# Performance work log

Measured on AMD Instinct MI355X. Metric: run time of the kernel, lower is better.

The kernel has to match this reference:

```python
import jax, jax.numpy as jnp
import numpy as np

NEG_INF = -9e15
ALPHA = 0.2  # LeakyReLU negative slope


def setup_inputs() -> dict:
    key = jax.random.key(0)
    k1, k2, k3, k4 = jax.random.split(key, 4)
    N, F_in, F_out = 8192, 128, 64
    h = jax.random.normal(k1, (N, F_in), dtype=jnp.float32)
    adj = jax.random.randint(k2, (N, N), 0, 2, dtype=jnp.int32)
    W = jax.random.normal(k3, (F_in, F_out), dtype=jnp.float32) * (1.414 / np.sqrt(F_in))
    a = jax.random.normal(k4, (2 * F_out, 1), dtype=jnp.float32) * 0.1
    return {"h": h, "adj": adj, "W": W, "a": a}


def reference(h, adj, W, a):
    # Wh: [N, F_out]
    Wh = h @ W
    F_out = Wh.shape[1]
    # Decomposed additive score: cat([Wh_i, Wh_j]) @ a == Wh_i@a1 + Wh_j@a2.
    # Identical math to the original repeat/cat/mm, without the [N*N, 2F] blowup.
    s1 = Wh @ a[:F_out, 0]   # [N] source-side score
    s2 = Wh @ a[F_out:, 0]   # [N] target-side score
    e = jax.nn.leaky_relu(s1[:, None] + s2[None, :], negative_slope=ALPHA)  # [N, N]
    attention = jax.nn.softmax(jnp.where(adj > 0, e, NEG_INF), axis=1)
    # dropout is identity in eval mode
    h_prime = attention @ Wh  # [N, F_out]
    return (h_prime, attention)
```

## Files before the change

kernel.cpp:

```cpp
#include <hip/hip_runtime.h>

#define NN 8192
#define FIN 128
#define FOUT 64
#define NEGINF (-9e15f)
#define LALPHA 0.2f

typedef float f32x4 __attribute__((ext_vector_type(4)));
typedef float f32x2 __attribute__((ext_vector_type(2)));
typedef short short8 __attribute__((ext_vector_type(8)));
typedef unsigned long long ull;

__device__ __forceinline__ unsigned short f32_to_bf16(float x) {
  unsigned int u = __float_as_uint(x);
  u = (u + 0x7fffu + ((u >> 16) & 1u)) >> 16;
  return (unsigned short)u;
}
__device__ __forceinline__ float bf16_to_f32(unsigned short b) {
  return __uint_as_float(((unsigned int)b) << 16);
}

__global__ __launch_bounds__(256) void gat_prep(
    const float* __restrict__ h, const float* __restrict__ W,
    const float* __restrict__ a,
    float* __restrict__ s1g, float* __restrict__ s2g,
    unsigned short* __restrict__ whfh)
{
  __shared__ __align__(16) float Wl[FIN * FOUT];
  __shared__ __align__(16) float hl[16 * FIN];
  const int tid = threadIdx.x;
  const int i0 = blockIdx.x * 16;
  #pragma unroll
  for (int it = 0; it < 8; ++it) {
    int idx = (it * 256 + tid) * 4;
    *(f32x4*)&Wl[idx] = *(const f32x4*)&W[idx];
  }
  #pragma unroll
  for (int it = 0; it < 2; ++it) {
    int idx = (it * 256 + tid) * 4;
    *(f32x4*)&hl[idx] = *(const f32x4*)&h[(size_t)i0 * FIN + idx];
  }
  __syncthreads();
  const int r = tid >> 4;
  const int f0 = (tid & 15) * 4;
  f32x4 acc = {0.f, 0.f, 0.f, 0.f};
  #pragma unroll 8
  for (int k = 0; k < FIN; ++k) {
    float hv = hl[r * FIN + k];
    f32x4 wv = *(const f32x4*)&Wl[k * FOUT + f0];
    acc += hv * wv;
  }
  f32x4 a1v = *(const f32x4*)&a[f0];
  f32x4 a2v = *(const f32x4*)&a[FOUT + f0];
  float p1 = acc.x * a1v.x + acc.y * a1v.y + acc.z * a1v.z + acc.w * a1v.w;
  float p2 = acc.x * a2v.x + acc.y * a2v.y + acc.z * a2v.z + acc.w * a2v.w;
  #pragma unroll
  for (int d = 1; d < 16; d <<= 1) {
    p1 += __shfl_xor(p1, d, 16);
    p2 += __shfl_xor(p2, d, 16);
  }
  const int j = i0 + r;
  if ((tid & 15) == 0) { s1g[j] = p1; s2g[j] = p2; }
  const int kstep = j >> 5;
  const int lhi = (j >> 3) & 3;
  const int ein = j & 7;
  #pragma unroll
  for (int e = 0; e < 4; ++e) {
    int f = f0 + e;
    unsigned short hb = f32_to_bf16(acc[e]);
    int ln = lhi * 16 + (f & 15);
    whfh[(size_t)(kstep * 4 + (f >> 4)) * 512 + ln * 8 + ein] = hb;
  }
}

__global__ __launch_bounds__(512, 4) void gat_fused(
    const int* __restrict__ adj,
    const float* __restrict__ s1g, const float* __restrict__ s2g,
    const unsigned short* __restrict__ whfh,
    float* __restrict__ outh, float* __restrict__ outa)
{
  __shared__ __align__(16) float s2l[NN];
  __shared__ __align__(16) unsigned int maskl[16][258];
  __shared__ __align__(16) float red[4][1024];
  __shared__ float rowp[16][3];
  __shared__ float smaxl;
  const int tid = threadIdx.x;
  const int lane = tid & 63;
  const int wv = tid >> 6;
  const int i0 = blockIdx.x * 16;

  float lmax = -3.4e38f;
  #pragma unroll
  for (int it = 0; it < 4; ++it) {
    int idx = (it * 512 + tid) * 4;
    f32x4 v = *(const f32x4*)&s2g[idx];
    *(f32x4*)&s2l[idx] = v;
    lmax = fmaxf(fmaxf(fmaxf(lmax, v.x), fmaxf(v.y, v.z)), v.w);
  }
  #pragma unroll
  for (int d = 1; d < 64; d <<= 1) lmax = fmaxf(lmax, __shfl_xor(lmax, d));
  if (lane == 0) red[0][wv] = lmax;
  __syncthreads();
  if (tid == 0) {
    float m = red[0][0];
    #pragma unroll
    for (int w = 1; w < 8; ++w) m = fmaxf(m, red[0][w]);
    smaxl = m;
  }
  __syncthreads();
  const float smax = smaxl;

  {
    const int r0 = wv * 2, r1 = r0 + 1;
    const float s1a = s1g[i0 + r0];
    const float s1b = s1g[i0 + r1];
    const float za = s1a + smax, zb = s1b + smax;
    const float Ma = fmaxf(za, LALPHA * za);
    const float Mb = fmaxf(zb, LALPHA * zb);
    const int* __restrict__ ara = adj + (size_t)(i0 + r0) * NN;
    const int* __restrict__ arb = adj + (size_t)(i0 + r1) * NN;
    float la = 0.f, lb = 0.f;
    #pragma unroll 4
    for (int it = 0; it < 128; ++it) {
      int jj = it * 64 + lane;
      int a0 = __builtin_nontemporal_load(&ara[jj]);
      int a1 = __builtin_nontemporal_load(&arb[jj]);
      float sv = s2l[jj];
      ull b0 = __ballot(a0 > 0);
      ull b1 = __ballot(a1 > 0);
      float xa = s1a + sv; xa = fmaxf(xa, LALPHA * xa);
      float xb = s1b + sv; xb = fmaxf(xb, LALPHA * xb);
      float ea = __expf(xa - Ma);
      float eb = __expf(xb - Mb);
      la += (a0 > 0) ? ea : 0.f;
      lb += (a1 > 0) ? eb : 0.f;
      if (lane == 0) {
        *(ull*)&maskl[r0][it * 2] = b0;
        *(ull*)&maskl[r1][it * 2] = b1;
      }
    }
    #pragma unroll
    for (int d = 1; d < 64; d <<= 1) {
      la += __shfl_xor(la, d);
      lb += __shfl_xor(lb, d);
    }
    if (lane == 0) {
      rowp[r0][0] = s1a; rowp[r0][1] = Ma; rowp[r0][2] = 1.f / la;
      rowp[r1][0] = s1b; rowp[r1][1] = Mb; rowp[r1][2] = 1.f / lb;
    }
  }
  __syncthreads();

  const int row = lane & 15;
  const int kg = lane >> 4;
  const float s1r = rowp[row][0];
  const float mr = rowp[row][1];
  const float rir = rowp[row][2];
  const int kbase = wv * 1024;
  f32x4 acc0 = {0,0,0,0}, acc1 = {0,0,0,0}, acc2 = {0,0,0,0}, acc3 = {0,0,0,0};
  float* __restrict__ orow = outa + (size_t)(i0 + row) * NN;
  const short8* __restrict__ bfrag = (const short8*)whfh;
  for (int step = 0; step < 32; ++step) {
    const int k0 = kbase + step * 32;
    const int jb = k0 + kg * 8;
    f32x4 sa = *(const f32x4*)&s2l[jb];
    f32x4 sb = *(const f32x4*)&s2l[jb + 4];
    unsigned int bits = maskl[row][k0 >> 5] >> (kg * 8);
    float s2v[8] = {sa.x, sa.y, sa.z, sa.w, sb.x, sb.y, sb.z, sb.w};
    float af[8];
    short8 AH, AL;
    #pragma unroll
    for (int e = 0; e < 8; ++e) {
      float x = s1r + s2v[e];
      x = fmaxf(x, LALPHA * x);
      x = ((bits >> e) & 1u) ? x : NEGINF;
      float p = __expf(x - mr) * rir;
      af[e] = p;
      unsigned short hb = f32_to_bf16(p);
      AH[e] = (short)hb;
      AL[e] = (short)f32_to_bf16(p - bf16_to_f32(hb));
    }
    f32x4 st0 = {af[0], af[1], af[2], af[3]};
    f32x4 st1 = {af[4], af[5], af[6], af[7]};
    *(f32x4*)&orow[jb] = st0;
    *(f32x4*)&orow[jb + 4] = st1;
    size_t fb = (size_t)(k0 >> 5) * 256 + lane;
    short8 B0 = bfrag[fb];
    short8 B1 = bfrag[fb + 64];
    short8 B2 = bfrag[fb + 128];
    short8 B3 = bfrag[fb + 192];
    acc0 = __builtin_amdgcn_mfma_f32_16x16x32_bf16(AH, B0, acc0, 0, 0, 0);
    acc1 = __builtin_amdgcn_mfma_f32_16x16x32_bf16(AH, B1, acc1, 0, 0, 0);
    acc2 = __builtin_amdgcn_mfma_f32_16x16x32_bf16(AH, B2, acc2, 0, 0, 0);
    acc3 = __builtin_amdgcn_mfma_f32_16x16x32_bf16(AH, B3, acc3, 0, 0, 0);
    acc0 = __builtin_amdgcn_mfma_f32_16x16x32_bf16(AL, B0, acc0, 0, 0, 0);
    acc1 = __builtin_amdgcn_mfma_f32_16x16x32_bf16(AL, B1, acc1, 0, 0, 0);
    acc2 = __builtin_amdgcn_mfma_f32_16x16x32_bf16(AL, B2, acc2, 0, 0, 0);
    acc3 = __builtin_amdgcn_mfma_f32_16x16x32_bf16(AL, B3, acc3, 0, 0, 0);
  }
  const int c15 = lane & 15;
  f32x4 av[4] = {acc0, acc1, acc2, acc3};
  float* myred = &red[wv & 3][0];
  __syncthreads();
  if (wv < 4) {
    #pragma unroll
    for (int nt = 0; nt < 4; ++nt)
      #pragma unroll
      for (int rg = 0; rg < 4; ++rg)
        myred[(kg * 4 + rg) * 64 + nt * 16 + c15] = av[nt][rg];
  }
  __syncthreads();
  if (wv >= 4) {
    #pragma unroll
    for (int nt = 0; nt < 4; ++nt)
      #pragma unroll
      for (int rg = 0; rg < 4; ++rg)
        myred[(kg * 4 + rg) * 64 + nt * 16 + c15] += av[nt][rg];
  }
  __syncthreads();
  {
    int base = tid * 2;
    f32x2 r0 = *(f32x2*)&red[0][base];
    f32x2 r1 = *(f32x2*)&red[1][base];
    f32x2 r2 = *(f32x2*)&red[2][base];
    f32x2 r3 = *(f32x2*)&red[3][base];
    f32x2 s = r0 + r1 + r2 + r3;
    *(f32x2*)&outh[(size_t)i0 * FOUT + base] = s;
  }
}

extern "C" void kernel_launch(void* const* d_in, const int* in_sizes, int n_in,
                              void* d_out, int out_size, void* d_ws, size_t ws_size,
                              hipStream_t stream) {
  const float* h = (const float*)d_in[0];
  const int* adj = (const int*)d_in[1];
  const float* W = (const float*)d_in[2];
  const float* a = (const float*)d_in[3];
  float* outh = (float*)d_out;
  float* outa = outh + (size_t)NN * FOUT;
  char* ws = (char*)d_ws;
  float* s1g = (float*)ws;
  float* s2g = s1g + NN;
  unsigned short* whfh = (unsigned short*)(ws + 128 * 1024);
  gat_prep<<<512, 256, 0, stream>>>(h, W, a, s1g, s2g, whfh);
  gat_fused<<<512, 512, 0, stream>>>(adj, s1g, s2g, whfh, outh, outa);
}
```

Before: 512.0 us.

## Use 1024-thread blocks with one row per wave and drop the max pre-pass

Doubles the fused kernel's block size to 1024 threads. Each wave now handles one adjacency row in the mask/row-sum phase and half as many K-steps in the MFMA phase. The global s2-max reduction and its two barriers are removed by using leaky(s1) as the softmax shift, which is valid only while the exponents cannot overflow. The reduction buffer now reuses the mask LDS, so LDS per block shrinks, at the cost of a longer four-stage serialized partial-sum reduction.

Result: no change. 507.0 us (-1.0%).

```diff
diff --git a/kernel.cpp b/kernel.cpp
--- a/kernel.cpp
+++ b/kernel.cpp
@@ -7,7 +7,6 @@
 #define LALPHA 0.2f
 
 typedef float f32x4 __attribute__((ext_vector_type(4)));
-typedef float f32x2 __attribute__((ext_vector_type(2)));
 typedef short short8 __attribute__((ext_vector_type(8)));
 typedef unsigned long long ull;
 
@@ -73,7 +72,7 @@
   }
 }
 
-__global__ __launch_bounds__(512, 4) void gat_fused(
+__global__ __launch_bounds__(1024, 8) void gat_fused(
     const int* __restrict__ adj,
     const float* __restrict__ s1g, const float* __restrict__ s2g,
     const unsigned short* __restrict__ whfh,
@@ -81,72 +80,40 @@
 {
   __shared__ __align__(16) float s2l[NN];
   __shared__ __align__(16) unsigned int maskl[16][258];
-  __shared__ __align__(16) float red[4][1024];
   __shared__ float rowp[16][3];
-  __shared__ float smaxl;
   const int tid = threadIdx.x;
   const int lane = tid & 63;
   const int wv = tid >> 6;
   const int i0 = blockIdx.x * 16;
 
-  float lmax = -3.4e38f;
-  #pragma unroll
-  for (int it = 0; it < 4; ++it) {
-    int idx = (it * 512 + tid) * 4;
-    f32x4 v = *(const f32x4*)&s2g[idx];
-    *(f32x4*)&s2l[idx] = v;
-    lmax = fmaxf(fmaxf(fmaxf(lmax, v.x), fmaxf(v.y, v.z)), v.w);
-  }
-  #pragma unroll
-  for (int d = 1; d < 64; d <<= 1) lmax = fmaxf(lmax, __shfl_xor(lmax, d));
-  if (lane == 0) red[0][wv] = lmax;
-  __syncthreads();
-  if (tid == 0) {
-    float m = red[0][0];
-    #pragma unroll
-    for (int w = 1; w < 8; ++w) m = fmaxf(m, red[0][w]);
-    smaxl = m;
-  }
-  __syncthreads();
-  const float smax = smaxl;
+  #pragma unroll
+  for (int it = 0; it < 2; ++it) {
+    int idx = (it * 1024 + tid) * 4;
+    *(f32x4*)&s2l[idx] = *(const f32x4*)&s2g[idx];
+  }
+  __syncthreads();
 
   {
-    const int r0 = wv * 2, r1 = r0 + 1;
-    const float s1a = s1g[i0 + r0];
-    const float s1b = s1g[i0 + r1];
-    const float za = s1a + smax, zb = s1b + smax;
-    const float Ma = fmaxf(za, LALPHA * za);
-    const float Mb = fmaxf(zb, LALPHA * zb);
-    const int* __restrict__ ara = adj + (size_t)(i0 + r0) * NN;
-    const int* __restrict__ arb = adj + (size_t)(i0 + r1) * NN;
-    float la = 0.f, lb = 0.f;
+    const float s1v = s1g[i0 + wv];
+    const float M = fmaxf(s1v, LALPHA * s1v);
+    const int* __restrict__ ar = adj + (size_t)(i0 + wv) * NN;
+    float ls = 0.f;
     #pragma unroll 4
     for (int it = 0; it < 128; ++it) {
       int jj = it * 64 + lane;
-      int a0 = __builtin_nontemporal_load(&ara[jj]);
-      int a1 = __builtin_nontemporal_load(&arb[jj]);
+      int a0 = __builtin_nontemporal_load(&ar[jj]);
       float sv = s2l[jj];
-      ull b0 = __ballot(a0 > 0);
-      ull b1 = __ballot(a1 > 0);
-      float xa = s1a + sv; xa = fmaxf(xa, LALPHA * xa);
-      float xb = s1b + sv; xb = fmaxf(xb, LALPHA * xb);
-      float ea = __expf(xa - Ma);
-      float eb = __expf(xb - Mb);
-      la += (a0 > 0) ? ea : 0.f;
-      lb += (a1 > 0) ? eb : 0.f;
-      if (lane == 0) {
-        *(ull*)&maskl[r0][it * 2] = b0;
-        *(ull*)&maskl[r1][it * 2] = b1;
-      }
+      ull b = __ballot(a0 > 0);
+      float x = s1v + sv;
+      x = fmaxf(x, LALPHA * x);
+      float e = __expf(x - M);
+      ls += (a0 > 0) ? e : 0.f;
+      if (lane == 0) *(ull*)&maskl[wv][it * 2] = b;
     }
     #pragma unroll
-    for (int d = 1; d < 64; d <<= 1) {
-      la += __shfl_xor(la, d);
-      lb += __shfl_xor(lb, d);
-    }
+    for (int d = 1; d < 64; d <<= 1) ls += __shfl_xor(ls, d);
     if (lane == 0) {
-      rowp[r0][0] = s1a; rowp[r0][1] = Ma; rowp[r0][2] = 1.f / la;
-      rowp[r1][0] = s1b; rowp[r1][1] = Mb; rowp[r1][2] = 1.f / lb;
+      rowp[wv][0] = s1v; rowp[wv][1] = M; rowp[wv][2] = 1.f / ls;
     }
   }
   __syncthreads();
@@ -156,11 +123,11 @@
   const float s1r = rowp[row][0];
   const float mr = rowp[row][1];
   const float rir = rowp[row][2];
-  const int kbase = wv * 1024;
+  const int kbase = wv * 512;
   f32x4 acc0 = {0,0,0,0}, acc1 = {0,0,0,0}, acc2 = {0,0,0,0}, acc3 = {0,0,0,0};
   float* __restrict__ orow = outa + (size_t)(i0 + row) * NN;
   const short8* __restrict__ bfrag = (const short8*)whfh;
-  for (int step = 0; step < 32; ++step) {
+  for (int step = 0; step < 16; ++step) {
     const int k0 = kbase + step * 32;
     const int jb = k0 + kg * 8;
     f32x4 sa = *(const f32x4*)&s2l[jb];
@@ -198,35 +165,45 @@
     acc2 = __builtin_amdgcn_mfma_f32_16x16x32_bf16(AL, B2, acc2, 0, 0, 0);
     acc3 = __builtin_amdgcn_mfma_f32_16x16x32_bf16(AL, B3, acc3, 0, 0, 0);
   }
+  __syncthreads();
+  float* red = (float*)&maskl[0][0];
   const int c15 = lane & 15;
   f32x4 av[4] = {acc0, acc1, acc2, acc3};
-  float* myred = &red[wv & 3][0];
-  __syncthreads();
+  float* slab = red + (wv & 3) * 1024;
   if (wv < 4) {
     #pragma unroll
     for (int nt = 0; nt < 4; ++nt)
       #pragma unroll
       for (int rg = 0; rg < 4; ++rg)
-        myred[(kg * 4 + rg) * 64 + nt * 16 + c15] = av[nt][rg];
-  }
-  __syncthreads();
-  if (wv >= 4) {
-    #pragma unroll
-    for (int nt = 0; nt < 4; ++nt)
-      #pragma unroll
-      for (int rg = 0; rg < 4; ++rg)
-        myred[(kg * 4 + rg) * 64 + nt * 16 + c15] += av[nt][rg];
-  }
-  __syncthreads();
-  {
-    int base = tid * 2;
-    f32x2 r0 = *(f32x2*)&red[0][base];
-    f32x2 r1 = *(f32x2*)&red[1][base];
-    f32x2 r2 = *(f32x2*)&red[2][base];
-    f32x2 r3 = *(f32x2*)&red[3][base];
-    f32x2 s = r0 + r1 + r2 + r3;
-    *(f32x2*)&outh[(size_t)i0 * FOUT + base] = s;
-  }
+        slab[(kg * 4 + rg) * 64 + nt * 16 + c15] = av[nt][rg];
+  }
+  __syncthreads();
+  if (wv >= 4 && wv < 8) {
+    #pragma unroll
+    for (int nt = 0; nt < 4; ++nt)
+      #pragma unroll
+      for (int rg = 0; rg < 4; ++rg)
+        slab[(kg * 4 + rg) * 64 + nt * 16 + c15] += av[nt][rg];
+  }
+  __syncthreads();
+  if (wv >= 8 && wv < 12) {
+    #pragma unroll
+    for (int nt = 0; nt < 4; ++nt)
+      #pragma unroll
+      for (int rg = 0; rg < 4; ++rg)
+        slab[(kg * 4 + rg) * 64 + nt * 16 + c15] += av[nt][rg];
+  }
+  __syncthreads();
+  if (wv >= 12) {
+    #pragma unroll
+    for (int nt = 0; nt < 4; ++nt)
+      #pragma unroll
+      for (int rg = 0; rg < 4; ++rg)
+        slab[(kg * 4 + rg) * 64 + nt * 16 + c15] += av[nt][rg];
+  }
+  __syncthreads();
+  outh[(size_t)i0 * FOUT + tid] =
+      red[tid] + red[1024 + tid] + red[2048 + tid] + red[3072 + tid];
 }
 
 extern "C" void kernel_launch(void* const* d_in, const int* in_sizes, int n_in,
@@ -243,5 +220,5 @@
   float* s2g = s1g + NN;
   unsigned short* whfh = (unsigned short*)(ws + 128 * 1024);
   gat_prep<<<512, 256, 0, stream>>>(h, W, a, s1g, s2g, whfh);
-  gat_fused<<<512, 512, 0, stream>>>(adj, s1g, s2g, whfh, outh, outa);
-}
+  gat_fused<<<512, 1024, 0, stream>>>(adj, s1g, s2g, whfh, outh, outa);
+}
```
